# Optimization experiments

Measured on AMD Instinct MI355X. Metric: run time of the kernel, lower is better.

Reference implementation:

```python
import jax, jax.numpy as jnp
import numpy as np

B, S, D = 4, 2048, 1024  # batch, seq_len, d_emb (even for Givens pairs)


def givens_rotate(r, x):
    """Apply 2x2 Givens block rotations defined by r [D] to x [..., D]."""
    g = r.reshape(-1, 2)
    g = g / jnp.linalg.norm(g, axis=-1, keepdims=True)  # normalize (cos, sin) pairs
    xp = x.reshape(x.shape[:-1] + (x.shape[-1] // 2, 2))
    c, s = g[:, 0], g[:, 1]
    y0 = c * xp[..., 0] - s * xp[..., 1]
    y1 = c * xp[..., 1] + s * xp[..., 0]
    return jnp.stack([y0, y1], axis=-1).reshape(x.shape)


def setup_inputs() -> dict:
    key = jax.random.key(0)
    k1, k2 = jax.random.split(key, 2)
    Q = jax.random.normal(k1, (B, S, D), dtype=jnp.float32)
    # QKV_rotation.weight ~ U(-1, 1) per original init (before the identity overwrite)
    rot_w = jax.random.uniform(k2, (3, D), dtype=jnp.float32, minval=-1.0, maxval=1.0)
    scale = jnp.array([np.sqrt(D)], dtype=jnp.float32)
    bias = jnp.zeros((), dtype=jnp.float32)
    return {"Q": Q, "rot_w": rot_w, "scale": scale, "bias": bias}


def reference(Q, rot_w, scale, bias):
    # Givens-rotation 'projections' for q/k/v
    q = givens_rotate(rot_w[0], Q)
    k = givens_rotate(rot_w[1], Q)
    v = givens_rotate(rot_w[2], Q)
    # prepend zero time coordinate -> points on the Lorentz model ambient space
    zeros = jnp.zeros(Q.shape[:-1] + (1,), Q.dtype)
    q = jnp.concatenate([zeros, q], axis=-1)[:, None]  # [B,1,S,D+1]
    k = jnp.concatenate([zeros, k], axis=-1)[:, None]
    v = jnp.concatenate([zeros, v], axis=-1)[:, None]
    # Lorentz signature (-, +, +, ...)
    sgn = jnp.concatenate([-jnp.ones((1,), Q.dtype), jnp.ones((q.shape[-1] - 1,), Q.dtype)])
    # cinner(q, k): time-negated inner product -> scores [B,1,S,S]
    cin = jnp.einsum('bhqd,bhkd->bhqk', q * sgn, k)
    attn = jax.nn.softmax((2.0 + 2.0 * cin) / scale + bias, axis=-1)
    # Lorentz mid-point: weighted sum normalized by sqrt(|<m,m>_L|)
    ave = jnp.einsum('bhqk,bhkd->bhqd', attn, v)
    inner = jnp.sum(ave * ave * sgn, axis=-1, keepdims=True)
    denom = jnp.sqrt(jnp.clip(jnp.abs(inner), 1e-8, None))
    out = (ave / denom)[:, 0]  # [B,S,D+1]
    return out[..., 1:]  # drop time coordinate -> [B,S,D]
```

## Files before the change

kernel.cpp:

```cpp
#include <hip/hip_runtime.h>

typedef _Float16 h16;
typedef _Float16 half8 __attribute__((ext_vector_type(8)));
typedef _Float16 half4v __attribute__((ext_vector_type(4)));
typedef float floatx4 __attribute__((ext_vector_type(4)));

static constexpr int Bb_ = 4, S_ = 2048, D_ = 1024;

static __device__ __forceinline__ void gl_lds16(const void* g, void* l) {
  __builtin_amdgcn_global_load_lds(
      (const __attribute__((address_space(1))) unsigned int*)g,
      (__attribute__((address_space(3))) unsigned int*)l, 16, 0, 0);
}

static __device__ __forceinline__ void rot_pair(float q0, float q1, float a0,
                                                float a1, float b0, float b1,
                                                float c0, float c1, float& y0,
                                                float& y1, float& v0,
                                                float& v1) {
  float iqk = rsqrtf((a0 * a0 + a1 * a1) * (b0 * b0 + b1 * b1));
  float cc = (a0 * b0 + a1 * b1) * iqk;
  float ss = (a0 * b1 - a1 * b0) * iqk;
  y0 = cc * q0 - ss * q1;
  y1 = cc * q1 + ss * q0;
  float iv = rsqrtf(c0 * c0 + c1 * c1);
  float cv = c0 * iv, sv = c1 * iv;
  v0 = cv * q0 - sv * q1;
  v1 = cv * q1 + sv * q0;
}

__global__ __launch_bounds__(256) void k_prep_t(
    const float* __restrict__ Q, const float* __restrict__ rot,
    h16* __restrict__ Qh, h16* __restrict__ Kh, h16* __restrict__ VhT,
    float* __restrict__ pss, unsigned int* __restrict__ flags) {
  __shared__ __align__(16) h16 tile[64][64];
  int d0 = blockIdx.x * 64, s0 = blockIdx.y * 64, b = blockIdx.z;
  int t = threadIdx.x;
  int bl = blockIdx.x + 16 * (blockIdx.y + 32 * blockIdx.z);
  if (flags && bl == 0 && t < 32) flags[t] = 0u;
  if (pss && t < 4) pss[bl * 4 + t] = 0.f;
  const float* Qb = Q + ((size_t)b * S_ + s0) * D_ + d0;
  h16* Qhb = Qh + ((size_t)b * S_ + s0) * D_ + d0;
  h16* Khb = Kh + ((size_t)b * S_ + s0) * D_ + d0;
#pragma unroll
  for (int i = 0; i < 2; ++i) {
    int c = t + 256 * i;
    int row = c >> 3;
    int col = (c & 7) * 8;
    float4 qa = *(const float4*)&Qb[(size_t)row * D_ + col];
    float4 qb = *(const float4*)&Qb[(size_t)row * D_ + col + 4];
    int dg = (d0 + col) >> 2;
    float4 r0a = ((const float4*)rot)[dg];
    float4 r0b = ((const float4*)rot)[dg + 1];
    float4 r1a = ((const float4*)rot)[D_ / 4 + dg];
    float4 r1b = ((const float4*)rot)[D_ / 4 + dg + 1];
    float4 r2a = ((const float4*)rot)[2 * D_ / 4 + dg];
    float4 r2b = ((const float4*)rot)[2 * D_ / 4 + dg + 1];
    float y0, y1, y2, y3, y4, y5, y6, y7;
    float v0, v1, v2, v3, v4, v5, v6, v7;
    rot_pair(qa.x, qa.y, r0a.x, r0a.y, r1a.x, r1a.y, r2a.x, r2a.y, y0, y1, v0, v1);
    rot_pair(qa.z, qa.w, r0a.z, r0a.w, r1a.z, r1a.w, r2a.z, r2a.w, y2, y3, v2, v3);
    rot_pair(qb.x, qb.y, r0b.x, r0b.y, r1b.x, r1b.y, r2b.x, r2b.y, y4, y5, v4, v5);
    rot_pair(qb.z, qb.w, r0b.z, r0b.w, r1b.z, r1b.w, r2b.z, r2b.w, y6, y7, v6, v7);
    half8 qh = {(h16)qa.x, (h16)qa.y, (h16)qa.z, (h16)qa.w,
                (h16)qb.x, (h16)qb.y, (h16)qb.z, (h16)qb.w};
    half8 kh = {(h16)y0, (h16)y1, (h16)y2, (h16)y3,
                (h16)y4, (h16)y5, (h16)y6, (h16)y7};
    half8 vh = {(h16)v0, (h16)v1, (h16)v2, (h16)v3,
                (h16)v4, (h16)v5, (h16)v6, (h16)v7};
    *(half8*)&Qhb[(size_t)row * D_ + col] = qh;
    *(half8*)&Khb[(size_t)row * D_ + col] = kh;
    int pcol = col ^ ((row >> 3) << 3);
    *(half8*)&tile[row][pcol] = vh;
  }
  __syncthreads();
  h16* dst = VhT + ((size_t)b * D_ + d0) * S_ + s0;
#pragma unroll
  for (int i = 0; i < 2; ++i) {
    int c = t + 256 * i;
    int drow = c >> 3;
    int sc = (c & 7) * 8;
    int xr = sc;
    half8 v;
#pragma unroll
    for (int j = 0; j < 8; ++j) v[j] = tile[sc + j][drow ^ xr];
    *(half8*)&dst[(size_t)drow * S_ + sc] = v;
  }
}

#define G_FENCE asm volatile("" ::: "memory")
#define G_BAR                     \
  do {                            \
    G_FENCE;                      \
    __builtin_amdgcn_s_barrier(); \
    G_FENCE;                      \
  } while (0)

template <int NF, bool OUT16>
__global__ __launch_bounds__(512, 2) void k_gemm8(
    const char* __restrict__ A, int a_pitch, unsigned long long a_batch,
    const char* __restrict__ Bt, int b_pitch, unsigned long long b_batch,
    void* __restrict__ C, int c_pitch, unsigned long long c_batch, int Kdim,
    const float* __restrict__ scale_p, float* __restrict__ pss,
    unsigned int* __restrict__ flags) {
  constexpr int BNR = NF * 64;
  constexpr int JQ = NF / 2;
  __shared__ __align__(16) h16 As[2][2][256 * 32];
  __shared__ __align__(16) h16 Bs[2][2][BNR * 32];
  const int t = threadIdx.x;
  const int lane = t & 63;
  const int w = t >> 6;
  const int wm = (w >> 2) * 128;
  const int wn = (w & 3) * (NF * 16);
  const int id = blockIdx.x + 8 * (blockIdx.y + 8 * blockIdx.z);
  int tm, tn, tz, grp;
  if constexpr (OUT16) {
    const int L = (id & 7) * 32 + (id >> 3);
    tm = L & 7;
    tn = (L >> 3) & 7;
    tz = L >> 6;
    grp = 0;
  } else {
    const int xcd = id & 7, s2 = id >> 3;
    grp = xcd * 4 + (s2 >> 3);
    tn = s2 & 7;
    tz = grp >> 3;
    tm = grp & 7;
  }
  const char* Ab = A + (unsigned long long)tz * a_batch +
                   (unsigned long long)(tm * 256) * (unsigned long long)a_pitch;
  const char* Bb = Bt + (unsigned long long)tz * b_batch +
                   (unsigned long long)(tn * BNR) * (unsigned long long)b_pitch;
  const int srow = t >> 2;
  const int scol = ((t & 3) ^ ((t >> 3) & 3)) << 4;
  const int lds_o = t * 16;
  const int mrow = lane & 15, kc = lane >> 4;
  const int koff = (kc ^ ((mrow >> 1) & 3)) << 3;
  const int NT = Kdim >> 6;

#define SG_A(bf, kt, hm)                                                  \
  do {                                                                    \
    const char* sp_ = Ab +                                                \
                      (unsigned long long)(srow + (hm) * 128) * a_pitch + \
                      (kt) * 128 + scol;                                  \
    gl_lds16(sp_, (char*)&As[bf][0][(hm) * 128 * 32] + lds_o);            \
    gl_lds16(sp_ + 64, (char*)&As[bf][1][(hm) * 128 * 32] + lds_o);       \
  } while (0)
#define SG_B(bf, kt, hm)                                                  \
  do {                                                                    \
    const char* sp_ = Bb +                                                \
                      (unsigned long long)(srow + (hm) * 128) * b_pitch + \
                      (kt) * 128 + scol;                                  \
    gl_lds16(sp_, (char*)&Bs[bf][0][(hm) * 128 * 32] + lds_o);            \
    gl_lds16(sp_ + 64, (char*)&Bs[bf][1][(hm) * 128 * 32] + lds_o);       \
  } while (0)

  half8 ar0[4][2], ar1[4][2], br0[JQ][2], br1[JQ][2];
  floatx4 acc[8][NF];
#pragma unroll
  for (int i = 0; i < 8; ++i)
#pragma unroll
    for (int j = 0; j < NF; ++j) acc[i][j] = (floatx4){0.f, 0.f, 0.f, 0.f};

#define LDA_(bf, mh, DST)                                                \
  do {                                                                   \
    _Pragma("unroll") for (int i_ = 0; i_ < 4; ++i_) {                   \
      DST[i_][0] = *(const half8*)&As[bf][0]                             \
                       [(wm + ((mh) * 4 + i_) * 16 + mrow) * 32 + koff]; \
      DST[i_][1] = *(const half8*)&As[bf][1]                             \
                       [(wm + ((mh) * 4 + i_) * 16 + mrow) * 32 + koff]; \
    }                                                                    \
  } while (0)
#define LDB_(bf, nh, DST)                                                \
  do {                                                                   \
    _Pragma("unroll") for (int j_ = 0; j_ < JQ; ++j_) {                  \
      DST[j_][0] = *(const half8*)&Bs[bf][0]                             \
                       [(wn + ((nh)*JQ + j_) * 16 + mrow) * 32 + koff];  \
      DST[j_][1] = *(const half8*)&Bs[bf][1]                             \
                       [(wn + ((nh)*JQ + j_) * 16 + mrow) * 32 + koff];  \
    }                                                                    \
  } while (0)
#define QUAD(mh, nh, AF, BF)                                                 \
  do {                                                                       \
    __builtin_amdgcn_s_setprio(1);                                           \
    _Pragma("unroll") for (int i_ = 0; i_ < 4; ++i_)                         \
        _Pragma("unroll") for (int j_ = 0; j_ < JQ; ++j_) {                  \
      acc[(mh) * 4 + i_][(nh)*JQ + j_] =                                     \
          __builtin_amdgcn_mfma_f32_16x16x32_f16(                            \
              AF[i_][0], BF[j_][0], acc[(mh) * 4 + i_][(nh)*JQ + j_], 0, 0,  \
              0);                                                            \
      acc[(mh) * 4 + i_][(nh)*JQ + j_] =                                     \
          __builtin_amdgcn_mfma_f32_16x16x32_f16(                            \
              AF[i_][1], BF[j_][1], acc[(mh) * 4 + i_][(nh)*JQ + j_], 0, 0,  \
              0);                                                            \
    }                                                                        \
    __builtin_amdgcn_s_setprio(0);                                           \
  } while (0)

  SG_A(0, 0, 0);
  SG_A(0, 0, 1);
  SG_B(0, 0, 0);
  if constexpr (NF == 4) SG_B(0, 0, 1);
  SG_B(1, 1, 0);
  if constexpr (NF == 4) SG_B(1, 1, 1);
  SG_A(1, 1, 0);
  if constexpr (NF == 4)
    asm volatile("s_waitcnt vmcnt(6)" ::: "memory");
  else
    asm volatile("s_waitcnt vmcnt(4)" ::: "memory");
  G_BAR;
  LDA_(0, 0, ar0);
  LDB_(0, 0, br0);

#define TILE_(bf, nb, u)                                   \
  do {                                                     \
    const int k1_ = ((u) + 1 < NT) ? (u) + 1 : NT - 1;     \
    const int k2_ = ((u) + 2 < NT) ? (u) + 2 : NT - 1;     \
                                                   \
    SG_A(nb, k1_, 1);                                      \
    G_BAR;                                                 \
    LDB_(bf, 1, br1);                                      \
    QUAD(0, 0, ar0, br0);                                  \
                                                   \
    G_BAR;                                                 \
    LDA_(bf, 1, ar1);                                      \
    QUAD(0, 1, ar0, br1);                                  \
                                                   \
    SG_B(bf, k2_, 0);                                      \
    G_BAR;                                                 \
    QUAD(1, 0, ar1, br0);                                  \
                                                   \
    if constexpr (NF == 4) SG_B(bf, k2_, 1);               \
    SG_A(bf, k2_, 0);                                      \
    if constexpr (NF == 4)                                 \
      asm volatile("s_waitcnt vmcnt(6)" ::: "memory");     \
    else                                                   \
      asm volatile("s_waitcnt vmcnt(4)" ::: "memory");     \
    G_BAR;                                                 \
    LDA_(nb, 0, ar0);  \
    LDB_(nb, 0, br0);                                      \
    QUAD(1, 1, ar1, br1);                                  \
  } while (0)

  for (int u = 0; u < NT; u += 2) {
    TILE_(0, 1, u);
    TILE_(1, 0, u + 1);
  }
  asm volatile("s_waitcnt vmcnt(0)" ::: "memory");

  const int m0 = tm * 256 + wm;
  const int n0 = tn * BNR + wn;
  const int ccol = lane & 15;
  const int rq = (lane >> 4) * 4;
  if constexpr (OUT16) {
    const float aexp = 2.0f / scale_p[0];
    h16* Cb = (h16*)C + (unsigned long long)tz * c_batch;
#pragma unroll
    for (int i = 0; i < 8; ++i)
#pragma unroll
      for (int j = 0; j < NF; ++j)
#pragma unroll
        for (int r = 0; r < 4; ++r)
          Cb[(unsigned long long)(m0 + i * 16 + rq + r) * c_pitch +
             (n0 + j * 16 + ccol)] = (h16)__expf(acc[i][j][r] * aexp - 8.0f);
  } else {
    float* Cb = (float*)C + (unsigned long long)tz * c_batch;
    if (pss) {
      __syncthreads();
      float* wsum = (float*)&As[0][0][0];
      float* finv = wsum + 4 * 256;
      float part[8][4];
#pragma unroll
      for (int i = 0; i < 8; ++i)
#pragma unroll
        for (int r = 0; r < 4; ++r) {
          float s = acc[i][0][r] * acc[i][0][r];
          if constexpr (NF > 1) s += acc[i][1][r] * acc[i][1][r];
#pragma unroll
          for (int m = 1; m < 16; m <<= 1) s += __shfl_xor(s, m);
          part[i][r] = s;
        }
      if ((lane & 15) == 0) {
#pragma unroll
        for (int i = 0; i < 8; ++i)
#pragma unroll
          for (int r = 0; r < 4; ++r)
            wsum[(w & 3) * 256 + wm + i * 16 + rq + r] = part[i][r];
      }
      __syncthreads();
      if (t < 256) {
        float s = wsum[t] + wsum[256 + t] + wsum[512 + t] + wsum[768 + t];
        __hip_atomic_fetch_add(&pss[(unsigned)grp * 256 + t], s,
                               __ATOMIC_RELAXED, __HIP_MEMORY_SCOPE_AGENT);
      }
      __syncthreads();
      if (t == 0) {
        __hip_atomic_fetch_add(&flags[grp], 1u, __ATOMIC_ACQ_REL,
                               __HIP_MEMORY_SCOPE_AGENT);
        while (__hip_atomic_load(&flags[grp], __ATOMIC_ACQUIRE,
                                 __HIP_MEMORY_SCOPE_AGENT) < 8u)
          __builtin_amdgcn_s_sleep(2);
      }
      __syncthreads();
      if (t < 256) {
        float ss2 = __hip_atomic_load(&pss[(unsigned)grp * 256 + t],
                                      __ATOMIC_RELAXED,
                                      __HIP_MEMORY_SCOPE_AGENT);
        finv[t] = rsqrtf(fmaxf(ss2, 1e-30f));
      }
      __syncthreads();
#pragma unroll
      for (int i = 0; i < 8; ++i) {
#pragma unroll
        for (int r = 0; r < 4; ++r) {
          const float f = finv[wm + i * 16 + rq + r];
#pragma unroll
          for (int j = 0; j < NF; ++j)
            Cb[(unsigned long long)(m0 + i * 16 + rq + r) * c_pitch +
               (n0 + j * 16 + ccol)] = acc[i][j][r] * f;
        }
      }
    } else {
#pragma unroll
      for (int i = 0; i < 8; ++i)
#pragma unroll
        for (int j = 0; j < NF; ++j)
#pragma unroll
          for (int r = 0; r < 4; ++r)
            Cb[(unsigned long long)(m0 + i * 16 + rq + r) * c_pitch +
               (n0 + j * 16 + ccol)] = acc[i][j][r];
    }
  }
#undef TILE_
#undef QUAD
#undef LDB_
#undef LDA_
#undef SG_B
#undef SG_A
}

__global__ __launch_bounds__(256) void k_epilogue(float* __restrict__ O) {
  int wv = threadIdx.x >> 6, ln = threadIdx.x & 63;
  int row = blockIdx.x * 4 + wv;
  float* base = O + (size_t)row * D_;
  float4 u[4];
#pragma unroll
  for (int r = 0; r < 4; ++r) u[r] = ((const float4*)base)[ln + 64 * r];
  float ss = 0.f;
#pragma unroll
  for (int r = 0; r < 4; ++r)
    ss += u[r].x * u[r].x + u[r].y * u[r].y + u[r].z * u[r].z + u[r].w * u[r].w;
#pragma unroll
  for (int off = 32; off; off >>= 1) ss += __shfl_xor(ss, off);
  float f = rsqrtf(fmaxf(ss, 1e-30f));
#pragma unroll
  for (int r = 0; r < 4; ++r) {
    float4 o;
    o.x = u[r].x * f;
    o.y = u[r].y * f;
    o.z = u[r].z * f;
    o.w = u[r].w * f;
    ((float4*)base)[ln + 64 * r] = o;
  }
}

extern "C" void kernel_launch(void* const* d_in, const int* in_sizes, int n_in,
                              void* d_out, int out_size, void* d_ws, size_t ws_size,
                              hipStream_t stream) {
  const float* Q = (const float*)d_in[0];
  const float* rot = (const float*)d_in[1];
  const float* scale = (const float*)d_in[2];
  float* O = (float*)d_out;
  char* ws = (char*)d_ws;
  const size_t MB = 1024ull * 1024ull;
  h16* Qh = (h16*)(ws);
  h16* Kh = (h16*)(ws + 16 * MB);
  h16* VhT = (h16*)(ws + 32 * MB);
  h16* Sl = (h16*)(ws + 48 * MB);
  float* pss = (float*)(ws + 80 * MB);
  unsigned int* flags = (unsigned int*)(ws + 80 * MB + 32 * 1024);
  const bool fused = ws_size >= 80 * MB + 32 * 1024 + 128;
  if (!fused) {
    pss = nullptr;
    flags = nullptr;
  }

  k_prep_t<<<dim3(D_ / 64, S_ / 64, Bb_), 256, 0, stream>>>(Q, rot, Qh, Kh,
                                                            VhT, pss, flags);
  k_gemm8<4, true><<<dim3(8, 8, 4), 512, 0, stream>>>(
      (const char*)Qh, D_ * 2, (unsigned long long)S_ * D_ * 2,
      (const char*)Kh, D_ * 2, (unsigned long long)S_ * D_ * 2,
      (void*)Sl, S_, (unsigned long long)S_ * S_, D_, scale, nullptr, nullptr);
  k_gemm8<2, false><<<dim3(8, 8, 4), 512, 0, stream>>>(
      (const char*)Sl, S_ * 2, (unsigned long long)S_ * S_ * 2,
      (const char*)VhT, S_ * 2, (unsigned long long)D_ * S_ * 2,
      (void*)O, D_, (unsigned long long)S_ * D_, S_, nullptr, pss, flags);
  if (!fused) k_epilogue<<<dim3(Bb_ * S_ / 4), 256, 0, stream>>>(O);
}
```

Before: 174.3 us.

## Fuse prep and both GEMMs into one persistent kernel with device barriers

Replaces the three kernel launches (prep/transpose, QK^T GEMM, PV GEMM) with a single persistent 256-block kernel. The stages are separated by a software grid-wide barrier built on an atomic ticket counter. The prep stage now loops over 8 tiles per block using 512 threads, and the non-fused fallback path is removed. This is meant to cut launch overhead and inter-kernel gaps, at the cost of a hipMemsetAsync per call. It also relies on all 256 blocks being co-resident, otherwise the barrier deadlocks.

```diff
diff --git a/kernel.cpp b/kernel.cpp
--- a/kernel.cpp
+++ b/kernel.cpp
@@ -2,7 +2,6 @@
 
 typedef _Float16 h16;
 typedef _Float16 half8 __attribute__((ext_vector_type(8)));
-typedef _Float16 half4v __attribute__((ext_vector_type(4)));
 typedef float floatx4 __attribute__((ext_vector_type(4)));
 
 static constexpr int Bb_ = 4, S_ = 2048, D_ = 1024;
@@ -29,64 +28,6 @@
   v1 = cv * q1 + sv * q0;
 }
 
-__global__ __launch_bounds__(256) void k_prep_t(
-    const float* __restrict__ Q, const float* __restrict__ rot,
-    h16* __restrict__ Qh, h16* __restrict__ Kh, h16* __restrict__ VhT,
-    float* __restrict__ pss, unsigned int* __restrict__ flags) {
-  __shared__ __align__(16) h16 tile[64][64];
-  int d0 = blockIdx.x * 64, s0 = blockIdx.y * 64, b = blockIdx.z;
-  int t = threadIdx.x;
-  int bl = blockIdx.x + 16 * (blockIdx.y + 32 * blockIdx.z);
-  if (flags && bl == 0 && t < 32) flags[t] = 0u;
-  if (pss && t < 4) pss[bl * 4 + t] = 0.f;
-  const float* Qb = Q + ((size_t)b * S_ + s0) * D_ + d0;
-  h16* Qhb = Qh + ((size_t)b * S_ + s0) * D_ + d0;
-  h16* Khb = Kh + ((size_t)b * S_ + s0) * D_ + d0;
-#pragma unroll
-  for (int i = 0; i < 2; ++i) {
-    int c = t + 256 * i;
-    int row = c >> 3;
-    int col = (c & 7) * 8;
-    float4 qa = *(const float4*)&Qb[(size_t)row * D_ + col];
-    float4 qb = *(const float4*)&Qb[(size_t)row * D_ + col + 4];
-    int dg = (d0 + col) >> 2;
-    float4 r0a = ((const float4*)rot)[dg];
-    float4 r0b = ((const float4*)rot)[dg + 1];
-    float4 r1a = ((const float4*)rot)[D_ / 4 + dg];
-    float4 r1b = ((const float4*)rot)[D_ / 4 + dg + 1];
-    float4 r2a = ((const float4*)rot)[2 * D_ / 4 + dg];
-    float4 r2b = ((const float4*)rot)[2 * D_ / 4 + dg + 1];
-    float y0, y1, y2, y3, y4, y5, y6, y7;
-    float v0, v1, v2, v3, v4, v5, v6, v7;
-    rot_pair(qa.x, qa.y, r0a.x, r0a.y, r1a.x, r1a.y, r2a.x, r2a.y, y0, y1, v0, v1);
-    rot_pair(qa.z, qa.w, r0a.z, r0a.w, r1a.z, r1a.w, r2a.z, r2a.w, y2, y3, v2, v3);
-    rot_pair(qb.x, qb.y, r0b.x, r0b.y, r1b.x, r1b.y, r2b.x, r2b.y, y4, y5, v4, v5);
-    rot_pair(qb.z, qb.w, r0b.z, r0b.w, r1b.z, r1b.w, r2b.z, r2b.w, y6, y7, v6, v7);
-    half8 qh = {(h16)qa.x, (h16)qa.y, (h16)qa.z, (h16)qa.w,
-                (h16)qb.x, (h16)qb.y, (h16)qb.z, (h16)qb.w};
-    half8 kh = {(h16)y0, (h16)y1, (h16)y2, (h16)y3,
-                (h16)y4, (h16)y5, (h16)y6, (h16)y7};
-    half8 vh = {(h16)v0, (h16)v1, (h16)v2, (h16)v3,
-                (h16)v4, (h16)v5, (h16)v6, (h16)v7};
-    *(half8*)&Qhb[(size_t)row * D_ + col] = qh;
-    *(half8*)&Khb[(size_t)row * D_ + col] = kh;
-    int pcol = col ^ ((row >> 3) << 3);
-    *(half8*)&tile[row][pcol] = vh;
-  }
-  __syncthreads();
-  h16* dst = VhT + ((size_t)b * D_ + d0) * S_ + s0;
-#pragma unroll
-  for (int i = 0; i < 2; ++i) {
-    int c = t + 256 * i;
-    int drow = c >> 3;
-    int sc = (c & 7) * 8;
-    int xr = sc;
-    half8 v;
-#pragma unroll
-    for (int j = 0; j < 8; ++j) v[j] = tile[sc + j][drow ^ xr];
-    *(half8*)&dst[(size_t)drow * S_ + sc] = v;
-  }
-}
 
 #define G_FENCE asm volatile("" ::: "memory")
 #define G_BAR                     \
@@ -96,32 +37,98 @@
     G_FENCE;                      \
   } while (0)
 
+static __device__ __forceinline__ void dev_barrier(unsigned int* bar, int t) {
+  __syncthreads();
+  if (t == 0) {
+    __threadfence();
+    unsigned int ticket = __hip_atomic_fetch_add(bar, 1u, __ATOMIC_ACQ_REL,
+                                                 __HIP_MEMORY_SCOPE_AGENT);
+    unsigned int target = (ticket / 256u + 1u) * 256u;
+    while ((int)(__hip_atomic_load(bar, __ATOMIC_ACQUIRE,
+                                   __HIP_MEMORY_SCOPE_AGENT) -
+                 target) < 0)
+      __builtin_amdgcn_s_sleep(2);
+    __threadfence();
+  }
+  __syncthreads();
+}
+
+#define AS_(bf, h) (as_base + ((bf)*2 + (h)) * 8192)
+#define BS_(bf, h) (bs_base + ((bf)*2 + (h)) * 8192)
+
+#define SG_A(bf, kt, hm)                                                  \
+  do {                                                                    \
+    const char* sp_ = Ab +                                                \
+                      (unsigned long long)(srow + (hm) * 128) * a_pitch + \
+                      (kt) * 128 + scol;                                  \
+    gl_lds16(sp_, (char*)(AS_(bf, 0) + (hm)*128 * 32) + lds_o);           \
+    gl_lds16(sp_ + 64, (char*)(AS_(bf, 1) + (hm)*128 * 32) + lds_o);      \
+  } while (0)
+#define SG_B(bf, kt, hm)                                                  \
+  do {                                                                    \
+    const char* sp_ = Bb +                                                \
+                      (unsigned long long)(srow + (hm) * 128) * b_pitch + \
+                      (kt) * 128 + scol;                                  \
+    gl_lds16(sp_, (char*)(BS_(bf, 0) + (hm)*128 * 32) + lds_o);           \
+    gl_lds16(sp_ + 64, (char*)(BS_(bf, 1) + (hm)*128 * 32) + lds_o);      \
+  } while (0)
+#define LDA_(bf, mh, DST)                                                   \
+  do {                                                                     \
+    _Pragma("unroll") for (int i_ = 0; i_ < 4; ++i_) {                     \
+      DST[i_][0] = *(const half8*)&AS_(                                    \
+          bf, 0)[(wm + ((mh)*4 + i_) * 16 + mrow) * 32 + koff];            \
+      DST[i_][1] = *(const half8*)&AS_(                                    \
+          bf, 1)[(wm + ((mh)*4 + i_) * 16 + mrow) * 32 + koff];            \
+    }                                                                      \
+  } while (0)
+#define LDB_(bf, nh, DST)                                                   \
+  do {                                                                     \
+    _Pragma("unroll") for (int j_ = 0; j_ < JQ; ++j_) {                    \
+      DST[j_][0] = *(const half8*)&BS_(                                    \
+          bf, 0)[(wn + ((nh)*JQ + j_) * 16 + mrow) * 32 + koff];           \
+      DST[j_][1] = *(const half8*)&BS_(                                    \
+          bf, 1)[(wn + ((nh)*JQ + j_) * 16 + mrow) * 32 + koff];           \
+    }                                                                      \
+  } while (0)
+#define QUAD(mh, nh, AF, BF)                                                \
+  do {                                                                      \
+    __builtin_amdgcn_s_setprio(1);                                          \
+    _Pragma("unroll") for (int i_ = 0; i_ < 4; ++i_)                        \
+        _Pragma("unroll") for (int j_ = 0; j_ < JQ; ++j_) {                 \
+      acc[(mh)*4 + i_][(nh)*JQ + j_] =                                      \
+          __builtin_amdgcn_mfma_f32_16x16x32_f16(                           \
+              AF[i_][0], BF[j_][0], acc[(mh)*4 + i_][(nh)*JQ + j_], 0, 0,   \
+              0);                                                           \
+      acc[(mh)*4 + i_][(nh)*JQ + j_] =                                      \
+          __builtin_amdgcn_mfma_f32_16x16x32_f16(                           \
+              AF[i_][1], BF[j_][1], acc[(mh)*4 + i_][(nh)*JQ + j_], 0, 0,   \
+              0);                                                           \
+    }                                                                       \
+    __builtin_amdgcn_s_setprio(0);                                          \
+  } while (0)
+
 template <int NF, bool OUT16>
-__global__ __launch_bounds__(512, 2) void k_gemm8(
-    const char* __restrict__ A, int a_pitch, unsigned long long a_batch,
-    const char* __restrict__ Bt, int b_pitch, unsigned long long b_batch,
-    void* __restrict__ C, int c_pitch, unsigned long long c_batch, int Kdim,
-    const float* __restrict__ scale_p, float* __restrict__ pss,
-    unsigned int* __restrict__ flags) {
+static __device__ __forceinline__ void gemm_body(
+    int blk, int t, h16* as_base, h16* bs_base, const char* __restrict__ A,
+    int a_pitch, unsigned long long a_batch, const char* __restrict__ Bt,
+    int b_pitch, unsigned long long b_batch, void* __restrict__ C, int c_pitch,
+    unsigned long long c_batch, int Kdim, const float* __restrict__ scale_p,
+    float* __restrict__ pss, unsigned int* __restrict__ flags) {
   constexpr int BNR = NF * 64;
   constexpr int JQ = NF / 2;
-  __shared__ __align__(16) h16 As[2][2][256 * 32];
-  __shared__ __align__(16) h16 Bs[2][2][BNR * 32];
-  const int t = threadIdx.x;
   const int lane = t & 63;
   const int w = t >> 6;
   const int wm = (w >> 2) * 128;
   const int wn = (w & 3) * (NF * 16);
-  const int id = blockIdx.x + 8 * (blockIdx.y + 8 * blockIdx.z);
   int tm, tn, tz, grp;
   if constexpr (OUT16) {
-    const int L = (id & 7) * 32 + (id >> 3);
+    const int L = (blk & 7) * 32 + (blk >> 3);
     tm = L & 7;
     tn = (L >> 3) & 7;
     tz = L >> 6;
     grp = 0;
   } else {
-    const int xcd = id & 7, s2 = id >> 3;
+    const int xcd = blk & 7, s2 = blk >> 3;
     grp = xcd * 4 + (s2 >> 3);
     tn = s2 & 7;
     tz = grp >> 3;
@@ -138,64 +145,12 @@
   const int koff = (kc ^ ((mrow >> 1) & 3)) << 3;
   const int NT = Kdim >> 6;
 
-#define SG_A(bf, kt, hm)                                                  \
-  do {                                                                    \
-    const char* sp_ = Ab +                                                \
-                      (unsigned long long)(srow + (hm) * 128) * a_pitch + \
-                      (kt) * 128 + scol;                                  \
-    gl_lds16(sp_, (char*)&As[bf][0][(hm) * 128 * 32] + lds_o);            \
-    gl_lds16(sp_ + 64, (char*)&As[bf][1][(hm) * 128 * 32] + lds_o);       \
-  } while (0)
-#define SG_B(bf, kt, hm)                                                  \
-  do {                                                                    \
-    const char* sp_ = Bb +                                                \
-                      (unsigned long long)(srow + (hm) * 128) * b_pitch + \
-                      (kt) * 128 + scol;                                  \
-    gl_lds16(sp_, (char*)&Bs[bf][0][(hm) * 128 * 32] + lds_o);            \
-    gl_lds16(sp_ + 64, (char*)&Bs[bf][1][(hm) * 128 * 32] + lds_o);       \
-  } while (0)
-
   half8 ar0[4][2], ar1[4][2], br0[JQ][2], br1[JQ][2];
   floatx4 acc[8][NF];
 #pragma unroll
   for (int i = 0; i < 8; ++i)
 #pragma unroll
     for (int j = 0; j < NF; ++j) acc[i][j] = (floatx4){0.f, 0.f, 0.f, 0.f};
-
-#define LDA_(bf, mh, DST)                                                \
-  do {                                                                   \
-    _Pragma("unroll") for (int i_ = 0; i_ < 4; ++i_) {                   \
-      DST[i_][0] = *(const half8*)&As[bf][0]                             \
-                       [(wm + ((mh) * 4 + i_) * 16 + mrow) * 32 + koff]; \
-      DST[i_][1] = *(const half8*)&As[bf][1]                             \
-                       [(wm + ((mh) * 4 + i_) * 16 + mrow) * 32 + koff]; \
-    }                                                                    \
-  } while (0)
-#define LDB_(bf, nh, DST)                                                \
-  do {                                                                   \
-    _Pragma("unroll") for (int j_ = 0; j_ < JQ; ++j_) {                  \
-      DST[j_][0] = *(const half8*)&Bs[bf][0]                             \
-                       [(wn + ((nh)*JQ + j_) * 16 + mrow) * 32 + koff];  \
-      DST[j_][1] = *(const half8*)&Bs[bf][1]                             \
-                       [(wn + ((nh)*JQ + j_) * 16 + mrow) * 32 + koff];  \
-    }                                                                    \
-  } while (0)
-#define QUAD(mh, nh, AF, BF)                                                 \
-  do {                                                                       \
-    __builtin_amdgcn_s_setprio(1);                                           \
-    _Pragma("unroll") for (int i_ = 0; i_ < 4; ++i_)                         \
-        _Pragma("unroll") for (int j_ = 0; j_ < JQ; ++j_) {                  \
-      acc[(mh) * 4 + i_][(nh)*JQ + j_] =                                     \
-          __builtin_amdgcn_mfma_f32_16x16x32_f16(                            \
-              AF[i_][0], BF[j_][0], acc[(mh) * 4 + i_][(nh)*JQ + j_], 0, 0,  \
-              0);                                                            \
-      acc[(mh) * 4 + i_][(nh)*JQ + j_] =                                     \
-          __builtin_amdgcn_mfma_f32_16x16x32_f16(                            \
-              AF[i_][1], BF[j_][1], acc[(mh) * 4 + i_][(nh)*JQ + j_], 0, 0,  \
-              0);                                                            \
-    }                                                                        \
-    __builtin_amdgcn_s_setprio(0);                                           \
-  } while (0)
 
   SG_A(0, 0, 0);
   SG_A(0, 0, 1);
@@ -247,6 +202,7 @@
     TILE_(1, 0, u + 1);
   }
   asm volatile("s_waitcnt vmcnt(0)" ::: "memory");
+#undef TILE_
 
   const int m0 = tm * 256 + wm;
   const int n0 = tn * BNR + wn;
@@ -265,108 +221,148 @@
              (n0 + j * 16 + ccol)] = (h16)__expf(acc[i][j][r] * aexp - 8.0f);
   } else {
     float* Cb = (float*)C + (unsigned long long)tz * c_batch;
-    if (pss) {
-      __syncthreads();
-      float* wsum = (float*)&As[0][0][0];
-      float* finv = wsum + 4 * 256;
-      float part[8][4];
+    __syncthreads();
+    float* wsum = (float*)as_base;
+    float* finv = wsum + 4 * 256;
+    float part[8][4];
+#pragma unroll
+    for (int i = 0; i < 8; ++i)
+#pragma unroll
+      for (int r = 0; r < 4; ++r) {
+        float s = acc[i][0][r] * acc[i][0][r];
+        if constexpr (NF > 1) s += acc[i][1][r] * acc[i][1][r];
+#pragma unroll
+        for (int m = 1; m < 16; m <<= 1) s += __shfl_xor(s, m);
+        part[i][r] = s;
+      }
+    if ((lane & 15) == 0) {
 #pragma unroll
       for (int i = 0; i < 8; ++i)
 #pragma unroll
-        for (int r = 0; r < 4; ++r) {
-          float s = acc[i][0][r] * acc[i][0][r];
-          if constexpr (NF > 1) s += acc[i][1][r] * acc[i][1][r];
-#pragma unroll
-          for (int m = 1; m < 16; m <<= 1) s += __shfl_xor(s, m);
-          part[i][r] = s;
-        }
-      if ((lane & 15) == 0) {
-#pragma unroll
-        for (int i = 0; i < 8; ++i)
-#pragma unroll
-          for (int r = 0; r < 4; ++r)
-            wsum[(w & 3) * 256 + wm + i * 16 + rq + r] = part[i][r];
+        for (int r = 0; r < 4; ++r)
+          wsum[(w & 3) * 256 + wm + i * 16 + rq + r] = part[i][r];
+    }
+    __syncthreads();
+    if (t < 256) {
+      float s = wsum[t] + wsum[256 + t] + wsum[512 + t] + wsum[768 + t];
+      __hip_atomic_fetch_add(&pss[(unsigned)grp * 256 + t], s,
+                             __ATOMIC_RELAXED, __HIP_MEMORY_SCOPE_AGENT);
+    }
+    __syncthreads();
+    if (t == 0) {
+      __hip_atomic_fetch_add(&flags[grp], 1u, __ATOMIC_ACQ_REL,
+                             __HIP_MEMORY_SCOPE_AGENT);
+      while (__hip_atomic_load(&flags[grp], __ATOMIC_ACQUIRE,
+                               __HIP_MEMORY_SCOPE_AGENT) < 8u)
+        __builtin_amdgcn_s_sleep(2);
+    }
+    __syncthreads();
+    if (t < 256) {
+      float ss2 = __hip_atomic_load(&pss[(unsigned)grp * 256 + t],
+                                    __ATOMIC_RELAXED, __HIP_MEMORY_SCOPE_AGENT);
+      finv[t] = rsqrtf(fmaxf(ss2, 1e-30f));
+    }
+    __syncthreads();
+#pragma unroll
+    for (int i = 0; i < 8; ++i) {
+#pragma unroll
+      for (int r = 0; r < 4; ++r) {
+        const float f = finv[wm + i * 16 + rq + r];
+#pragma unroll
+        for (int j = 0; j < NF; ++j)
+          Cb[(unsigned long long)(m0 + i * 16 + rq + r) * c_pitch +
+             (n0 + j * 16 + ccol)] = acc[i][j][r] * f;
       }
-      __syncthreads();
-      if (t < 256) {
-        float s = wsum[t] + wsum[256 + t] + wsum[512 + t] + wsum[768 + t];
-        __hip_atomic_fetch_add(&pss[(unsigned)grp * 256 + t], s,
-                               __ATOMIC_RELAXED, __HIP_MEMORY_SCOPE_AGENT);
-      }
-      __syncthreads();
-      if (t == 0) {
-        __hip_atomic_fetch_add(&flags[grp], 1u, __ATOMIC_ACQ_REL,
-                               __HIP_MEMORY_SCOPE_AGENT);
-        while (__hip_atomic_load(&flags[grp], __ATOMIC_ACQUIRE,
-                                 __HIP_MEMORY_SCOPE_AGENT) < 8u)
-          __builtin_amdgcn_s_sleep(2);
-      }
-      __syncthreads();
-      if (t < 256) {
-        float ss2 = __hip_atomic_load(&pss[(unsigned)grp * 256 + t],
-                                      __ATOMIC_RELAXED,
-                                      __HIP_MEMORY_SCOPE_AGENT);
-        finv[t] = rsqrtf(fmaxf(ss2, 1e-30f));
-      }
-      __syncthreads();
-#pragma unroll
-      for (int i = 0; i < 8; ++i) {
-#pragma unroll
-        for (int r = 0; r < 4; ++r) {
-          const float f = finv[wm + i * 16 + rq + r];
-#pragma unroll
-          for (int j = 0; j < NF; ++j)
-            Cb[(unsigned long long)(m0 + i * 16 + rq + r) * c_pitch +
-               (n0 + j * 16 + ccol)] = acc[i][j][r] * f;
-        }
-      }
-    } else {
-#pragma unroll
-      for (int i = 0; i < 8; ++i)
-#pragma unroll
-        for (int j = 0; j < NF; ++j)
-#pragma unroll
-          for (int r = 0; r < 4; ++r)
-            Cb[(unsigned long long)(m0 + i * 16 + rq + r) * c_pitch +
-               (n0 + j * 16 + ccol)] = acc[i][j][r];
-    }
-  }
-#undef TILE_
-#undef QUAD
-#undef LDB_
-#undef LDA_
-#undef SG_B
-#undef SG_A
-}
-
-__global__ __launch_bounds__(256) void k_epilogue(float* __restrict__ O) {
-  int wv = threadIdx.x >> 6, ln = threadIdx.x & 63;
-  int row = blockIdx.x * 4 + wv;
-  float* base = O + (size_t)row * D_;
-  float4 u[4];
-#pragma unroll
-  for (int r = 0; r < 4; ++r) u[r] = ((const float4*)base)[ln + 64 * r];
-  float ss = 0.f;
-#pragma unroll
-  for (int r = 0; r < 4; ++r)
-    ss += u[r].x * u[r].x + u[r].y * u[r].y + u[r].z * u[r].z + u[r].w * u[r].w;
-#pragma unroll
-  for (int off = 32; off; off >>= 1) ss += __shfl_xor(ss, off);
-  float f = rsqrtf(fmaxf(ss, 1e-30f));
-#pragma unroll
-  for (int r = 0; r < 4; ++r) {
-    float4 o;
-    o.x = u[r].x * f;
-    o.y = u[r].y * f;
-    o.z = u[r].z * f;
-    o.w = u[r].w * f;
-    ((float4*)base)[ln + 64 * r] = o;
-  }
+    }
+  }
+}
+
+__global__ __launch_bounds__(512, 2) void k_mega(
+    const float* __restrict__ Q, const float* __restrict__ rot,
+    h16* __restrict__ Qh, h16* __restrict__ Kh, h16* __restrict__ VhT,
+    h16* __restrict__ Sl, float* __restrict__ O,
+    const float* __restrict__ scale_p, float* __restrict__ pss,
+    unsigned int* __restrict__ flags, unsigned int* __restrict__ bar) {
+  __shared__ __align__(16) h16 AsS[2][2][256 * 32];
+  __shared__ __align__(16) h16 BsS[2][2][256 * 32];
+  h16* as_base = &AsS[0][0][0];
+  h16* bs_base = &BsS[0][0][0];
+  const int blk = blockIdx.x;
+  const int t = threadIdx.x;
+
+  if (t < 32) pss[blk * 32 + t] = 0.f;
+  if (blk == 0 && t < 32) flags[t] = 0u;
+  h16* tile = as_base;
+  for (int it = 0; it < 8; ++it) {
+    const int gid = blk * 8 + it;
+    const int d0 = (gid & 15) * 64, s0 = ((gid >> 4) & 31) * 64, b = gid >> 9;
+    const float* Qb = Q + ((size_t)b * S_ + s0) * D_ + d0;
+    h16* Qhb = Qh + ((size_t)b * S_ + s0) * D_ + d0;
+    h16* Khb = Kh + ((size_t)b * S_ + s0) * D_ + d0;
+    {
+      const int row = t >> 3;
+      const int col = (t & 7) * 8;
+      float4 qa = *(const float4*)&Qb[(size_t)row * D_ + col];
+      float4 qb = *(const float4*)&Qb[(size_t)row * D_ + col + 4];
+      const int dg = (d0 + col) >> 2;
+      float4 r0a = ((const float4*)rot)[dg];
+      float4 r0b = ((const float4*)rot)[dg + 1];
+      float4 r1a = ((const float4*)rot)[D_ / 4 + dg];
+      float4 r1b = ((const float4*)rot)[D_ / 4 + dg + 1];
+      float4 r2a = ((const float4*)rot)[2 * D_ / 4 + dg];
+      float4 r2b = ((const float4*)rot)[2 * D_ / 4 + dg + 1];
+      float y0, y1, y2, y3, y4, y5, y6, y7;
+      float v0, v1, v2, v3, v4, v5, v6, v7;
+      rot_pair(qa.x, qa.y, r0a.x, r0a.y, r1a.x, r1a.y, r2a.x, r2a.y, y0, y1,
+               v0, v1);
+      rot_pair(qa.z, qa.w, r0a.z, r0a.w, r1a.z, r1a.w, r2a.z, r2a.w, y2, y3,
+               v2, v3);
+      rot_pair(qb.x, qb.y, r0b.x, r0b.y, r1b.x, r1b.y, r2b.x, r2b.y, y4, y5,
+               v4, v5);
+      rot_pair(qb.z, qb.w, r0b.z, r0b.w, r1b.z, r1b.w, r2b.z, r2b.w, y6, y7,
+               v6, v7);
+      half8 qh = {(h16)qa.x, (h16)qa.y, (h16)qa.z, (h16)qa.w,
+                  (h16)qb.x, (h16)qb.y, (h16)qb.z, (h16)qb.w};
+      half8 kh = {(h16)y0, (h16)y1, (h16)y2, (h16)y3,
+                  (h16)y4, (h16)y5, (h16)y6, (h16)y7};
+      half8 vh = {(h16)v0, (h16)v1, (h16)v2, (h16)v3,
+                  (h16)v4, (h16)v5, (h16)v6, (h16)v7};
+      *(half8*)&Qhb[(size_t)row * D_ + col] = qh;
+      *(half8*)&Khb[(size_t)row * D_ + col] = kh;
+      const int pcol = col ^ ((row >> 3) << 3);
+      *(half8*)&tile[row * 64 + pcol] = vh;
+    }
+    __syncthreads();
+    {
+      h16* dst = VhT + ((size_t)b * D_ + d0) * S_ + s0;
+      const int drow = t >> 3;
+      const int sc = (t & 7) * 8;
+      const int xr = sc;
+      half8 v;
+#pragma unroll
+      for (int j = 0; j < 8; ++j) v[j] = tile[(sc + j) * 64 + (drow ^ xr)];
+      *(half8*)&dst[(size_t)drow * S_ + sc] = v;
+    }
+    __syncthreads();
+  }
+
+  dev_barrier(bar, t);
+  gemm_body<4, true>(blk, t, as_base, bs_base, (const char*)Qh, D_ * 2,
+                     (unsigned long long)S_ * D_ * 2, (const char*)Kh, D_ * 2,
+                     (unsigned long long)S_ * D_ * 2, (void*)Sl, S_,
+                     (unsigned long long)S_ * S_, D_, scale_p, nullptr,
+                     nullptr);
+
+  dev_barrier(bar, t);
+  gemm_body<2, false>(blk, t, as_base, bs_base, (const char*)Sl, S_ * 2,
+                      (unsigned long long)S_ * S_ * 2, (const char*)VhT,
+                      S_ * 2, (unsigned long long)D_ * S_ * 2, (void*)O, D_,
+                      (unsigned long long)S_ * D_, S_, nullptr, pss, flags);
 }
 
 extern "C" void kernel_launch(void* const* d_in, const int* in_sizes, int n_in,
-                              void* d_out, int out_size, void* d_ws, size_t ws_size,
-                              hipStream_t stream) {
+                              void* d_out, int out_size, void* d_ws,
+                              size_t ws_size, hipStream_t stream) {
   const float* Q = (const float*)d_in[0];
   const float* rot = (const float*)d_in[1];
   const float* scale = (const float*)d_in[2];
@@ -379,21 +375,8 @@
   h16* Sl = (h16*)(ws + 48 * MB);
   float* pss = (float*)(ws + 80 * MB);
   unsigned int* flags = (unsigned int*)(ws + 80 * MB + 32 * 1024);
-  const bool fused = ws_size >= 80 * MB + 32 * 1024 + 128;
-  if (!fused) {
-    pss = nullptr;
-    flags = nullptr;
-  }
-
-  k_prep_t<<<dim3(D_ / 64, S_ / 64, Bb_), 256, 0, stream>>>(Q, rot, Qh, Kh,
-                                                            VhT, pss, flags);
-  k_gemm8<4, true><<<dim3(8, 8, 4), 512, 0, stream>>>(
-      (const char*)Qh, D_ * 2, (unsigned long long)S_ * D_ * 2,
-      (const char*)Kh, D_ * 2, (unsigned long long)S_ * D_ * 2,
-      (void*)Sl, S_, (unsigned long long)S_ * S_, D_, scale, nullptr, nullptr);
-  k_gemm8<2, false><<<dim3(8, 8, 4), 512, 0, stream>>>(
-      (const char*)Sl, S_ * 2, (unsigned long long)S_ * S_ * 2,
-      (const char*)VhT, S_ * 2, (unsigned long long)D_ * S_ * 2,
-      (void*)O, D_, (unsigned long long)S_ * D_, S_, nullptr, pss, flags);
-  if (!fused) k_epilogue<<<dim3(Bb_ * S_ / 4), 256, 0, stream>>>(O);
-}
+  unsigned int* bar = (unsigned int*)(ws + 80 * MB + 33 * 1024);
+  hipMemsetAsync(bar, 0, 64, stream);
+  k_mega<<<dim3(256), 512, 0, stream>>>(Q, rot, Qh, Kh, VhT, Sl, O, scale, pss,
+                                        flags, bar);
+}
```

Result: slower. 268.4 us (+54.0%).
